# Kernel optimization log

Measured on AMD Instinct MI355X. Metric: run time of the kernel, lower is better.

## Reference

```python
import jax, jax.numpy as jnp
import numpy as np

X_LB, X_UB = 0.0, 25.0  # module-level normalization bounds (time domain)


def _lstm_layer(x, h0, c0, Wih, Whh, bih, bhh):
    """Unbatched PyTorch-style LSTM layer. x: [T, in], returns h seq [T, H].
    Gate order i, f, g, o; gates = x@Wih.T + bih + h@Whh.T + bhh."""
    gx = x @ Wih.T + (bih + bhh)  # [T, 4H] precomputed input contribution

    def step(carry, g):
        h, c = carry
        i, f, gg, o = jnp.split(g + h @ Whh.T, 4)
        c = jax.nn.sigmoid(f) * c + jax.nn.sigmoid(i) * jnp.tanh(gg)
        h = jax.nn.sigmoid(o) * jnp.tanh(c)
        return (h, c), h

    _, hs = jax.lax.scan(step, (h0, c0), gx)
    return hs


def setup_inputs() -> dict:
    key = jax.random.key(0)
    ks = jax.random.split(key, 17)
    T, H1, H2 = 200000, 32, 3

    def u(k, shape, fan):  # torch LSTM default init: U(-1/sqrt(H), 1/sqrt(H))
        s = 1.0 / np.sqrt(fan)
        return jax.random.uniform(k, shape, jnp.float32, -s, s)

    return {
        "x": jax.random.uniform(ks[0], (T, 1), jnp.float32, 0.0, 25.0),
        "pre_Wih0": u(ks[1], (4 * H1, 1), H1),
        "pre_Whh0": u(ks[2], (4 * H1, H1), H1),
        "pre_bih0": u(ks[3], (4 * H1,), H1),
        "pre_bhh0": u(ks[4], (4 * H1,), H1),
        "pre_Wih1": u(ks[5], (4 * H1, H1), H1),
        "pre_Whh1": u(ks[6], (4 * H1, H1), H1),
        "pre_bih1": u(ks[7], (4 * H1,), H1),
        "pre_bhh1": u(ks[8], (4 * H1,), H1),
        "pre_h0": jax.random.normal(ks[9], (2, H1), jnp.float32),
        "pre_c0": jax.random.normal(ks[10], (2, H1), jnp.float32),
        "post_Wih": u(ks[11], (4 * H2, H1), H2),
        "post_Whh": u(ks[12], (4 * H2, H2), H2),
        "post_bih": u(ks[13], (4 * H2,), H2),
        "post_bhh": u(ks[14], (4 * H2,), H2),
        "post_h0": jax.random.normal(ks[15], (1, H2), jnp.float32),
        "post_c0": jax.random.normal(ks[16], (1, H2), jnp.float32),
    }


def reference(x, pre_Wih0, pre_Whh0, pre_bih0, pre_bhh0,
              pre_Wih1, pre_Whh1, pre_bih1, pre_bhh1, pre_h0, pre_c0,
              post_Wih, post_Whh, post_bih, post_bhh, post_h0, post_c0):
    xn = (x - X_LB) / (X_UB - X_LB)                      # input normalization
    h = _lstm_layer(xn, pre_h0[0], pre_c0[0], pre_Wih0, pre_Whh0, pre_bih0, pre_bhh0)
    h = _lstm_layer(h, pre_h0[1], pre_c0[1], pre_Wih1, pre_Whh1, pre_bih1, pre_bhh1)
    out = _lstm_layer(h, post_h0[0], post_c0[0], post_Wih, post_Whh, post_bih, post_bhh)
    return out  # [T, 3]
```

## Files before the change

kernel.cpp:

```cpp
#include <hip/hip_runtime.h>
#include <cstddef>


#define XCH 256
#define SPB 8

typedef float f32x2 __attribute__((ext_vector_type(2)));
typedef float f32x4 __attribute__((ext_vector_type(4)));

__device__ __forceinline__ f32x2 pk_fma(f32x2 a, f32x2 b, f32x2 c) {
    f32x2 d;
    asm("v_pk_fma_f32 %0, %1, %2, %3" : "=v"(d) : "v"(a), "v"(b), "v"(c));
    return d;
}
__device__ __forceinline__ f32x4 lds_ld4(const float* p) {
    f32x4 v; __builtin_memcpy(&v, p, sizeof(f32x4)); return v;
}
__device__ __forceinline__ f32x2 lo2(f32x4 v) { f32x2 r; r[0] = v[0]; r[1] = v[1]; return r; }
__device__ __forceinline__ f32x2 hi2(f32x4 v) { f32x2 r; r[0] = v[2]; r[1] = v[3]; return r; }

__device__ __forceinline__ float v_exp2(float x) {
    float r; asm("v_exp_f32 %0, %1" : "=v"(r) : "v"(x)); return r;
}
__device__ __forceinline__ float v_rcp(float x) {
    float r; asm("v_rcp_f32 %0, %1" : "=v"(r) : "v"(x)); return r;
}
__device__ __forceinline__ float fast_gate_k(float x, float kl2e, float kl2e_lo,
                                             float m, float a0) {
    const float LN2 = 0.69314718055994530942f;
    const float t  = x * kl2e;
    const float r  = fmaf(x, kl2e, -t);
    const float dt = fmaf(x, kl2e_lo, r);
    const float e0 = v_exp2(t);
    const float e  = fmaf(e0, dt * LN2, e0);
    return fmaf(m, v_rcp(1.0f + e), a0);
}
#define KT   (-2.88539004325866699218750f)
#define KT_LO (-3.8519259822e-8f)
__device__ __forceinline__ float fast_tanh(float c) {
    return fast_gate_k(c, KT, KT_LO, 2.0f, -1.0f);
}
#define K1   (-1.44269502162933349609375f)
#define K1_LO (-1.9259629911e-8f)

__device__ __forceinline__ float swap1(float v) {
    return __shfl_xor(v, 1);
}

__device__ __forceinline__ void pipe_barrier() {
    asm volatile("s_waitcnt lgkmcnt(0)\n\ts_barrier" ::: "memory");
}

__global__ __launch_bounds__(256, 1)
void lstm3_r12_kernel(const float* __restrict__ x,
                      const float* __restrict__ Wih0, const float* __restrict__ Whh0,
                      const float* __restrict__ bih0, const float* __restrict__ bhh0,
                      const float* __restrict__ Wih1, const float* __restrict__ Whh1,
                      const float* __restrict__ bih1, const float* __restrict__ bhh1,
                      const float* __restrict__ pre_h0, const float* __restrict__ pre_c0,
                      const float* __restrict__ Wih2, const float* __restrict__ Whh2,
                      const float* __restrict__ bih2, const float* __restrict__ bhh2,
                      const float* __restrict__ post_h0, const float* __restrict__ post_c0,
                      float* __restrict__ out, int T)
{
    const int tid = threadIdx.x;
    const int w   = tid >> 6;
    const int l   = tid & 63;

    __shared__ __align__(16) float h0s[2][SPB][32];
    __shared__ __align__(16) float h1s[2][SPB][32];
    __shared__ __align__(16) float u1s[2][SPB][128];
    __shared__ __align__(16) float xbuf[2][XCH];

    const int T8   = (T + SPB - 1) / SPB;
    const int Etot = T8 + 3;

    if (w == 0) {
        const int cell = l >> 1, hf = l & 1;
        const int rA = cell + (hf << 5);
        const int rB = rA + 64;
        const float wx0A = Wih0[rA];
        const float wx0B = Wih0[rB];
        const float b0A  = bih0[rA] + bhh0[rA];
        const float b0B  = bih0[rB] + bhh0[rB];
        f32x2 wA2[16], wB2[16];
#pragma unroll
        for (int r = 0; r < 16; ++r) {
            wA2[r][0] = Whh0[rA * 32 + 2 * r]; wA2[r][1] = Whh0[rA * 32 + 2 * r + 1];
            wB2[r][0] = Whh0[rB * 32 + 2 * r]; wB2[r][1] = Whh0[rB * 32 + 2 * r + 1];
        }
        const float klB   = (hf == 0) ? KT    : K1;
        const float klBlo = (hf == 0) ? KT_LO : K1_LO;
        const float mB    = (hf == 0) ?  2.0f :  1.0f;
        const float a0B   = (hf == 0) ? -1.0f :  0.0f;

        float c0 = 0.0f;
        if (hf == 0) { c0 = pre_c0[cell]; h0s[1][SPB - 1][cell] = pre_h0[cell]; }
        __syncthreads();

        for (int e = 0; e < Etot; ++e) {
#pragma unroll
            for (int j = 0; j < SPB; ++j) {
                const int t = SPB * e + j;
                const float xn = xbuf[(t >> 8) & 1][t & (XCH - 1)];
                const float* hp = (j == 0) ? h0s[(e + 1) & 1][SPB - 1]
                                           : h0s[e & 1][j - 1];
                f32x2 aA0, aA1, aB0, aB1;
                aA0[0] = fmaf(xn, wx0A, b0A); aA0[1] = 0.0f;
                aA1[0] = 0.0f;                aA1[1] = 0.0f;
                aB0[0] = fmaf(xn, wx0B, b0B); aB0[1] = 0.0f;
                aB1[0] = 0.0f;                aB1[1] = 0.0f;
#pragma unroll
                for (int q = 0; q < 4; ++q) {
                    const f32x4 ha = lds_ld4(&hp[q * 8]);
                    const f32x4 hb = lds_ld4(&hp[q * 8 + 4]);
                    aA0 = pk_fma(lo2(ha), wA2[4 * q],     aA0);
                    aA1 = pk_fma(hi2(ha), wA2[4 * q + 1], aA1);
                    aB0 = pk_fma(lo2(ha), wB2[4 * q],     aB0);
                    aB1 = pk_fma(hi2(ha), wB2[4 * q + 1], aB1);
                    aA0 = pk_fma(lo2(hb), wA2[4 * q + 2], aA0);
                    aA1 = pk_fma(hi2(hb), wA2[4 * q + 3], aA1);
                    aB0 = pk_fma(lo2(hb), wB2[4 * q + 2], aB0);
                    aB1 = pk_fma(hi2(hb), wB2[4 * q + 3], aB1);
                }
                const float sA = (aA0[0] + aA0[1]) + (aA1[0] + aA1[1]);
                const float sB = (aB0[0] + aB0[1]) + (aB1[0] + aB1[1]);
                const float actA = fast_gate_k(sA, K1, K1_LO, 1.0f, 0.0f);
                const float actB = fast_gate_k(sB, klB, klBlo, mB, a0B);
                const float foA = swap1(actA);
                const float foB = swap1(actB);
                if (hf == 0) {
                    c0 = fmaf(foA, c0, actA * actB);
                    h0s[e & 1][j][cell] = foB * fast_tanh(c0);
                }
            }
            pipe_barrier();
        }
    } else if (w == 1) {
        const int gA = l, gB = l + 64;
        const float b1A = bih1[gA] + bhh1[gA];
        f32x2 wA2[16], wB2[16];
#pragma unroll
        for (int r = 0; r < 16; ++r) {
            wA2[r][0] = Wih1[gA * 32 + 2 * r]; wA2[r][1] = Wih1[gA * 32 + 2 * r + 1];
            wB2[r][0] = Wih1[gB * 32 + 2 * r]; wB2[r][1] = Wih1[gB * 32 + 2 * r + 1];
        }
        __syncthreads();

        for (int e = 0; e < Etot; ++e) {
            if (e >= 1) {
#pragma unroll
                for (int j = 0; j < SPB; ++j) {
                    const float* hp = h0s[(e - 1) & 1][j];
                    f32x2 uA0, uA1, uB0, uB1;
                    uA0[0] = b1A;  uA0[1] = 0.0f;
                    uA1[0] = 0.0f; uA1[1] = 0.0f;
                    uB0[0] = 0.0f; uB0[1] = 0.0f;
                    uB1[0] = 0.0f; uB1[1] = 0.0f;
#pragma unroll
                    for (int q = 0; q < 4; ++q) {
                        const f32x4 ha = lds_ld4(&hp[q * 8]);
                        const f32x4 hb = lds_ld4(&hp[q * 8 + 4]);
                        uA0 = pk_fma(lo2(ha), wA2[4 * q],     uA0);
                        uA1 = pk_fma(hi2(ha), wA2[4 * q + 1], uA1);
                        uB0 = pk_fma(lo2(ha), wB2[4 * q],     uB0);
                        uB1 = pk_fma(hi2(ha), wB2[4 * q + 1], uB1);
                        uA0 = pk_fma(lo2(hb), wA2[4 * q + 2], uA0);
                        uA1 = pk_fma(hi2(hb), wA2[4 * q + 3], uA1);
                        uB0 = pk_fma(lo2(hb), wB2[4 * q + 2], uB0);
                        uB1 = pk_fma(hi2(hb), wB2[4 * q + 3], uB1);
                    }
                    f32x2 up;
                    up[0] = (uA0[0] + uA0[1]) + (uA1[0] + uA1[1]);
                    up[1] = (uB0[0] + uB0[1]) + (uB1[0] + uB1[1]);
                    __builtin_memcpy(&u1s[e & 1][j][2 * l], &up, sizeof(f32x2));
                }
            }
            pipe_barrier();
        }
    } else if (w == 2) {
        const int cell = l >> 1, hf = l & 1;
        const int rA = cell + (hf << 5);
        const int rB = rA + 64;
        const float b1B = bih1[rB] + bhh1[rB];
        f32x2 wA2[16], wB2[16];
#pragma unroll
        for (int r = 0; r < 16; ++r) {
            wA2[r][0] = Whh1[rA * 32 + 2 * r]; wA2[r][1] = Whh1[rA * 32 + 2 * r + 1];
            wB2[r][0] = Whh1[rB * 32 + 2 * r]; wB2[r][1] = Whh1[rB * 32 + 2 * r + 1];
        }
        const float klB   = (hf == 0) ? KT    : K1;
        const float klBlo = (hf == 0) ? KT_LO : K1_LO;
        const float mB    = (hf == 0) ?  2.0f :  1.0f;
        const float a0B   = (hf == 0) ? -1.0f :  0.0f;

        float c1 = 0.0f;
        if (hf == 0) { c1 = pre_c0[32 + cell]; h1s[1][SPB - 1][cell] = pre_h0[32 + cell]; }
        __syncthreads();

        for (int e = 0; e < Etot; ++e) {
            if (e >= 2) {
#pragma unroll
                for (int j = 0; j < SPB; ++j) {
                    const float* gp = (j == 0) ? h1s[(e + 1) & 1][SPB - 1]
                                               : h1s[e & 1][j - 1];
                    const f32x4 ga0 = lds_ld4(&gp[0]);
                    const f32x4 gb0 = lds_ld4(&gp[4]);
                    f32x2 Up;
                    __builtin_memcpy(&Up, &u1s[(e - 1) & 1][j][2 * rA], sizeof(f32x2));
                    f32x2 vA0, vA1, vB0, vB1;
                    vA0[0] = 0.0f; vA0[1] = 0.0f;
                    vA1[0] = 0.0f; vA1[1] = 0.0f;
                    vB0[0] = b1B;  vB0[1] = 0.0f;
                    vB1[0] = 0.0f; vB1[1] = 0.0f;
                    vA0 = pk_fma(lo2(ga0), wA2[0], vA0);
                    vA1 = pk_fma(hi2(ga0), wA2[1], vA1);
                    vB0 = pk_fma(lo2(ga0), wB2[0], vB0);
                    vB1 = pk_fma(hi2(ga0), wB2[1], vB1);
                    vA0 = pk_fma(lo2(gb0), wA2[2], vA0);
                    vA1 = pk_fma(hi2(gb0), wA2[3], vA1);
                    vB0 = pk_fma(lo2(gb0), wB2[2], vB0);
                    vB1 = pk_fma(hi2(gb0), wB2[3], vB1);
#pragma unroll
                    for (int q = 1; q < 4; ++q) {
                        const f32x4 ga = lds_ld4(&gp[q * 8]);
                        const f32x4 gb = lds_ld4(&gp[q * 8 + 4]);
                        vA0 = pk_fma(lo2(ga), wA2[4 * q],     vA0);
                        vA1 = pk_fma(hi2(ga), wA2[4 * q + 1], vA1);
                        vB0 = pk_fma(lo2(ga), wB2[4 * q],     vB0);
                        vB1 = pk_fma(hi2(ga), wB2[4 * q + 1], vB1);
                        vA0 = pk_fma(lo2(gb), wA2[4 * q + 2], vA0);
                        vA1 = pk_fma(hi2(gb), wA2[4 * q + 3], vA1);
                        vB0 = pk_fma(lo2(gb), wB2[4 * q + 2], vB0);
                        vB1 = pk_fma(hi2(gb), wB2[4 * q + 3], vB1);
                    }
                    const float sA = Up[0] + ((vA0[0] + vA0[1]) + (vA1[0] + vA1[1]));
                    const float sB = Up[1] + ((vB0[0] + vB0[1]) + (vB1[0] + vB1[1]));
                    const float actA = fast_gate_k(sA, K1, K1_LO, 1.0f, 0.0f);
                    const float actB = fast_gate_k(sB, klB, klBlo, mB, a0B);
                    const float foA = swap1(actA);
                    const float foB = swap1(actB);
                    if (hf == 0) {
                        c1 = fmaf(foA, c1, actA * actB);
                        h1s[e & 1][j][cell] = foB * fast_tanh(c1);
                    }
                }
            }
            pipe_barrier();
        }
    } else {
        const int g2 = (l < 48) ? (l >> 2) : 0;
        const int p  = l & 3;
        f32x2 w2p[4];
#pragma unroll
        for (int r = 0; r < 4; ++r) {
            w2p[r][0] = Wih2[g2 * 32 + p * 8 + 2 * r];
            w2p[r][1] = Wih2[g2 * 32 + p * 8 + 2 * r + 1];
        }
        float wr2[3];
#pragma unroll
        for (int r = 0; r < 3; ++r) wr2[r] = Whh2[g2 * 3 + r];
        const float b2 = bih2[g2] + bhh2[g2];
        const bool  g2tanh = (g2 >= 6 && g2 <= 8);
        const float kl2   = g2tanh ? KT    : K1;
        const float kl2lo = g2tanh ? KT_LO : K1_LO;
        const float m2    = g2tanh ?  2.0f :  1.0f;
        const float a02   = g2tanh ? -1.0f :  0.0f;

        float c2 = 0.0f;
        if (l < 3) c2 = post_c0[l];
        float h2p0 = post_h0[0], h2p1 = post_h0[1], h2p2 = post_h0[2];
        float h2v = 0.0f;

        {
            const int i0 = 4 * l;
            if (i0 < T) {
                const float* xp = x + i0;
                float4 v;
                v.x = xp[0] / 25.0f;
                v.y = (i0 + 1 < T) ? xp[1] / 25.0f : 0.0f;
                v.z = (i0 + 2 < T) ? xp[2] / 25.0f : 0.0f;
                v.w = (i0 + 3 < T) ? xp[3] / 25.0f : 0.0f;
                __builtin_memcpy(&xbuf[0][i0], &v, sizeof(float4));
            }
        }
        __syncthreads();

        for (int e = 0; e < Etot; ++e) {
            if ((e & 31) == 0) {
                const int c = (e >> 5) + 1;
                const int base = c * XCH;
                if (base < T) {
                    const int i0 = base + 4 * l;
                    if (i0 < T) {
                        const float* xp = x + i0;
                        float4 v;
                        v.x = xp[0] / 25.0f;
                        v.y = (i0 + 1 < T) ? xp[1] / 25.0f : 0.0f;
                        v.z = (i0 + 2 < T) ? xp[2] / 25.0f : 0.0f;
                        v.w = (i0 + 3 < T) ? xp[3] / 25.0f : 0.0f;
                        __builtin_memcpy(&xbuf[c & 1][4 * l], &v, sizeof(float4));
                    }
                }
            }
            if (e >= 3) {
#pragma unroll
                for (int j = 0; j < SPB; ++j) {
                    const int t = SPB * (e - 3) + j;
                    const float* hp = h1s[(e - 1) & 1][j];
                    f32x2 acc; acc[0] = 0.0f; acc[1] = 0.0f;
                    {
                        const f32x4 ha = lds_ld4(&hp[p * 8 + 0]);
                        const f32x4 hb = lds_ld4(&hp[p * 8 + 4]);
                        acc = pk_fma(lo2(ha), w2p[0], acc);
                        acc = pk_fma(hi2(ha), w2p[1], acc);
                        acc = pk_fma(lo2(hb), w2p[2], acc);
                        acc = pk_fma(hi2(hb), w2p[3], acc);
                    }
                    float a2 = acc[0] + acc[1];
                    a2 += __shfl_xor(a2, 1);
                    a2 += __shfl_xor(a2, 2);
                    const float rec = fmaf(wr2[2], h2p2,
                                      fmaf(wr2[1], h2p1,
                                      fmaf(wr2[0], h2p0, b2)));
                    a2 += rec;
                    const float act2 = fast_gate_k(a2, kl2, kl2lo, m2, a02);
                    const int lj = (l < 3) ? l : 0;
                    const float i2  = __shfl(act2,  4 * lj);
                    const float f2  = __shfl(act2, 12 + 4 * lj);
                    const float g2v = __shfl(act2, 24 + 4 * lj);
                    const float o2  = __shfl(act2, 36 + 4 * lj);
                    if (l < 3) {
                        c2 = fmaf(f2, c2, i2 * g2v);
                        h2v = o2 * fast_tanh(c2);
                        if (t < T) out[(size_t)t * 3 + l] = h2v;
                    }
                    h2p0 = __shfl(h2v, 0);
                    h2p1 = __shfl(h2v, 1);
                    h2p2 = __shfl(h2v, 2);
                }
            }
            pipe_barrier();
        }
    }
}

extern "C" void kernel_launch(void* const* d_in, const int* in_sizes, int n_in,
                              void* d_out, int out_size, void* d_ws, size_t ws_size,
                              hipStream_t stream)
{
    const float* x       = (const float*)d_in[0];
    const float* Wih0    = (const float*)d_in[1];
    const float* Whh0    = (const float*)d_in[2];
    const float* bih0    = (const float*)d_in[3];
    const float* bhh0    = (const float*)d_in[4];
    const float* Wih1    = (const float*)d_in[5];
    const float* Whh1    = (const float*)d_in[6];
    const float* bih1    = (const float*)d_in[7];
    const float* bhh1    = (const float*)d_in[8];
    const float* pre_h0  = (const float*)d_in[9];
    const float* pre_c0  = (const float*)d_in[10];
    const float* Wih2    = (const float*)d_in[11];
    const float* Whh2    = (const float*)d_in[12];
    const float* bih2    = (const float*)d_in[13];
    const float* bhh2    = (const float*)d_in[14];
    const float* post_h0 = (const float*)d_in[15];
    const float* post_c0 = (const float*)d_in[16];

    const int T = in_sizes[0];

    lstm3_r12_kernel<<<dim3(1), dim3(256), 0, stream>>>(
        x, Wih0, Whh0, bih0, bhh0, Wih1, Whh1, bih1, bhh1, pre_h0, pre_c0,
        Wih2, Whh2, bih2, bhh2, post_h0, post_c0, (float*)d_out, T);
}
```

Before: 57.50 ms.

## Shorten LSTM recurrence critical path with wider accumulators, DPP gate gather, fused o*tanh

Several latency-oriented changes to the sequential single-block LSTM pipeline. Layer 0 and layer 1 now split their dot products across four packed accumulators instead of two, which shortens FMA dependency chains. Layer 0 loads eight x values per epoch with two vector LDS reads, and layer 1 hoists the u1s loads out of the step loop. The output layer is remapped so each of 12 lanes computes a full 32-wide dot product, replacing the cross-lane shuffle reduction and using DPP row shifts to gather gates. The o*tanh(c) product is folded into the final FMA; the DPP row-shift path relies on the 12 gates staying within one 16-lane row.

```diff
diff --git a/kernel.cpp b/kernel.cpp
--- a/kernel.cpp
+++ b/kernel.cpp
@@ -25,34 +25,52 @@
 __device__ __forceinline__ float v_rcp(float x) {
     float r; asm("v_rcp_f32 %0, %1" : "=v"(r) : "v"(x)); return r;
 }
+
+#define LN2F  0.69314718055994530942f
+#define KT    (-2.88539004325866699218750f)
+#define KT_LO (-3.8519259822e-8f)
+#define K1    (-1.44269502162933349609375f)
+#define K1_LO (-1.9259629911e-8f)
+
 __device__ __forceinline__ float fast_gate_k(float x, float kl2e, float kl2e_lo,
                                              float m, float a0) {
-    const float LN2 = 0.69314718055994530942f;
     const float t  = x * kl2e;
     const float r  = fmaf(x, kl2e, -t);
     const float dt = fmaf(x, kl2e_lo, r);
     const float e0 = v_exp2(t);
-    const float e  = fmaf(e0, dt * LN2, e0);
+    const float e  = fmaf(e0, dt * LN2F, e0);
     return fmaf(m, v_rcp(1.0f + e), a0);
 }
-#define KT   (-2.88539004325866699218750f)
-#define KT_LO (-3.8519259822e-8f)
-__device__ __forceinline__ float fast_tanh(float c) {
-    return fast_gate_k(c, KT, KT_LO, 2.0f, -1.0f);
-}
-#define K1   (-1.44269502162933349609375f)
-#define K1_LO (-1.9259629911e-8f)
+__device__ __forceinline__ float o_tanh(float o, float c) {
+    const float t  = c * KT;
+    const float r  = fmaf(c, KT, -t);
+    const float dt = fmaf(c, KT_LO, r);
+    const float e0 = v_exp2(t);
+    const float e  = fmaf(e0, dt * LN2F, e0);
+    const float s  = v_rcp(1.0f + e);
+    return fmaf(o + o, s, -o);
+}
 
 __device__ __forceinline__ float swap1(float v) {
     return __shfl_xor(v, 1);
 }
+template <int N>
+__device__ __forceinline__ float lane_plusN(float v) {
+#if __has_builtin(__builtin_amdgcn_update_dpp)
+    int i = __builtin_bit_cast(int, v);
+    i = __builtin_amdgcn_update_dpp(0, i, 0x100 + N, 0xF, 0xF, false);
+    return __builtin_bit_cast(float, i);
+#else
+    return __shfl_down(v, N);
+#endif
+}
 
 __device__ __forceinline__ void pipe_barrier() {
     asm volatile("s_waitcnt lgkmcnt(0)\n\ts_barrier" ::: "memory");
 }
 
 __global__ __launch_bounds__(256, 1)
-void lstm3_r12_kernel(const float* __restrict__ x,
+void lstm3_r14_kernel(const float* __restrict__ x,
                       const float* __restrict__ Wih0, const float* __restrict__ Whh0,
                       const float* __restrict__ bih0, const float* __restrict__ bhh0,
                       const float* __restrict__ Wih1, const float* __restrict__ Whh1,
@@ -99,39 +117,45 @@
         __syncthreads();
 
         for (int e = 0; e < Etot; ++e) {
+            const int t0 = SPB * e;
+            const float* xp = &xbuf[(t0 >> 8) & 1][t0 & (XCH - 1)];
+            const f32x4 xa = lds_ld4(xp);
+            const f32x4 xb = lds_ld4(xp + 4);
 #pragma unroll
             for (int j = 0; j < SPB; ++j) {
-                const int t = SPB * e + j;
-                const float xn = xbuf[(t >> 8) & 1][t & (XCH - 1)];
+                const float xn = (j < 4) ? xa[j] : xb[j - 4];
                 const float* hp = (j == 0) ? h0s[(e + 1) & 1][SPB - 1]
                                            : h0s[e & 1][j - 1];
-                f32x2 aA0, aA1, aB0, aB1;
-                aA0[0] = fmaf(xn, wx0A, b0A); aA0[1] = 0.0f;
-                aA1[0] = 0.0f;                aA1[1] = 0.0f;
-                aB0[0] = fmaf(xn, wx0B, b0B); aB0[1] = 0.0f;
-                aB1[0] = 0.0f;                aB1[1] = 0.0f;
+                f32x2 aA[4], aB[4];
+                aA[0][0] = fmaf(xn, wx0A, b0A); aA[0][1] = 0.0f;
+                aB[0][0] = fmaf(xn, wx0B, b0B); aB[0][1] = 0.0f;
+#pragma unroll
+                for (int s = 1; s < 4; ++s) { aA[s][0] = 0.0f; aA[s][1] = 0.0f;
+                                              aB[s][0] = 0.0f; aB[s][1] = 0.0f; }
 #pragma unroll
                 for (int q = 0; q < 4; ++q) {
                     const f32x4 ha = lds_ld4(&hp[q * 8]);
                     const f32x4 hb = lds_ld4(&hp[q * 8 + 4]);
-                    aA0 = pk_fma(lo2(ha), wA2[4 * q],     aA0);
-                    aA1 = pk_fma(hi2(ha), wA2[4 * q + 1], aA1);
-                    aB0 = pk_fma(lo2(ha), wB2[4 * q],     aB0);
-                    aB1 = pk_fma(hi2(ha), wB2[4 * q + 1], aB1);
-                    aA0 = pk_fma(lo2(hb), wA2[4 * q + 2], aA0);
-                    aA1 = pk_fma(hi2(hb), wA2[4 * q + 3], aA1);
-                    aB0 = pk_fma(lo2(hb), wB2[4 * q + 2], aB0);
-                    aB1 = pk_fma(hi2(hb), wB2[4 * q + 3], aB1);
-                }
-                const float sA = (aA0[0] + aA0[1]) + (aA1[0] + aA1[1]);
-                const float sB = (aB0[0] + aB0[1]) + (aB1[0] + aB1[1]);
+                    aA[0] = pk_fma(lo2(ha), wA2[4 * q],     aA[0]);
+                    aA[1] = pk_fma(hi2(ha), wA2[4 * q + 1], aA[1]);
+                    aA[2] = pk_fma(lo2(hb), wA2[4 * q + 2], aA[2]);
+                    aA[3] = pk_fma(hi2(hb), wA2[4 * q + 3], aA[3]);
+                    aB[0] = pk_fma(lo2(ha), wB2[4 * q],     aB[0]);
+                    aB[1] = pk_fma(hi2(ha), wB2[4 * q + 1], aB[1]);
+                    aB[2] = pk_fma(lo2(hb), wB2[4 * q + 2], aB[2]);
+                    aB[3] = pk_fma(hi2(hb), wB2[4 * q + 3], aB[3]);
+                }
+                const f32x2 sAv = (aA[0] + aA[1]) + (aA[2] + aA[3]);
+                const f32x2 sBv = (aB[0] + aB[1]) + (aB[2] + aB[3]);
+                const float sA = sAv[0] + sAv[1];
+                const float sB = sBv[0] + sBv[1];
                 const float actA = fast_gate_k(sA, K1, K1_LO, 1.0f, 0.0f);
                 const float actB = fast_gate_k(sB, klB, klBlo, mB, a0B);
                 const float foA = swap1(actA);
                 const float foB = swap1(actB);
                 if (hf == 0) {
                     c0 = fmaf(foA, c0, actA * actB);
-                    h0s[e & 1][j][cell] = foB * fast_tanh(c0);
+                    h0s[e & 1][j][cell] = o_tanh(foB, c0);
                 }
             }
             pipe_barrier();
@@ -200,72 +224,66 @@
 
         for (int e = 0; e < Etot; ++e) {
             if (e >= 2) {
+                f32x2 Up[SPB];
+#pragma unroll
+                for (int j = 0; j < SPB; ++j)
+                    __builtin_memcpy(&Up[j], &u1s[(e - 1) & 1][j][2 * rA], sizeof(f32x2));
 #pragma unroll
                 for (int j = 0; j < SPB; ++j) {
                     const float* gp = (j == 0) ? h1s[(e + 1) & 1][SPB - 1]
                                                : h1s[e & 1][j - 1];
-                    const f32x4 ga0 = lds_ld4(&gp[0]);
-                    const f32x4 gb0 = lds_ld4(&gp[4]);
-                    f32x2 Up;
-                    __builtin_memcpy(&Up, &u1s[(e - 1) & 1][j][2 * rA], sizeof(f32x2));
-                    f32x2 vA0, vA1, vB0, vB1;
-                    vA0[0] = 0.0f; vA0[1] = 0.0f;
-                    vA1[0] = 0.0f; vA1[1] = 0.0f;
-                    vB0[0] = b1B;  vB0[1] = 0.0f;
-                    vB1[0] = 0.0f; vB1[1] = 0.0f;
-                    vA0 = pk_fma(lo2(ga0), wA2[0], vA0);
-                    vA1 = pk_fma(hi2(ga0), wA2[1], vA1);
-                    vB0 = pk_fma(lo2(ga0), wB2[0], vB0);
-                    vB1 = pk_fma(hi2(ga0), wB2[1], vB1);
-                    vA0 = pk_fma(lo2(gb0), wA2[2], vA0);
-                    vA1 = pk_fma(hi2(gb0), wA2[3], vA1);
-                    vB0 = pk_fma(lo2(gb0), wB2[2], vB0);
-                    vB1 = pk_fma(hi2(gb0), wB2[3], vB1);
-#pragma unroll
-                    for (int q = 1; q < 4; ++q) {
+                    f32x2 vA[4], vB[4];
+                    vB[0][0] = b1B;  vB[0][1] = 0.0f;
+                    vA[0][0] = 0.0f; vA[0][1] = 0.0f;
+#pragma unroll
+                    for (int s = 1; s < 4; ++s) { vA[s][0] = 0.0f; vA[s][1] = 0.0f;
+                                                  vB[s][0] = 0.0f; vB[s][1] = 0.0f; }
+#pragma unroll
+                    for (int q = 0; q < 4; ++q) {
                         const f32x4 ga = lds_ld4(&gp[q * 8]);
                         const f32x4 gb = lds_ld4(&gp[q * 8 + 4]);
-                        vA0 = pk_fma(lo2(ga), wA2[4 * q],     vA0);
-                        vA1 = pk_fma(hi2(ga), wA2[4 * q + 1], vA1);
-                        vB0 = pk_fma(lo2(ga), wB2[4 * q],     vB0);
-                        vB1 = pk_fma(hi2(ga), wB2[4 * q + 1], vB1);
-                        vA0 = pk_fma(lo2(gb), wA2[4 * q + 2], vA0);
-                        vA1 = pk_fma(hi2(gb), wA2[4 * q + 3], vA1);
-                        vB0 = pk_fma(lo2(gb), wB2[4 * q + 2], vB0);
-                        vB1 = pk_fma(hi2(gb), wB2[4 * q + 3], vB1);
-                    }
-                    const float sA = Up[0] + ((vA0[0] + vA0[1]) + (vA1[0] + vA1[1]));
-                    const float sB = Up[1] + ((vB0[0] + vB0[1]) + (vB1[0] + vB1[1]));
+                        vA[0] = pk_fma(lo2(ga), wA2[4 * q],     vA[0]);
+                        vA[1] = pk_fma(hi2(ga), wA2[4 * q + 1], vA[1]);
+                        vA[2] = pk_fma(lo2(gb), wA2[4 * q + 2], vA[2]);
+                        vA[3] = pk_fma(hi2(gb), wA2[4 * q + 3], vA[3]);
+                        vB[0] = pk_fma(lo2(ga), wB2[4 * q],     vB[0]);
+                        vB[1] = pk_fma(hi2(ga), wB2[4 * q + 1], vB[1]);
+                        vB[2] = pk_fma(lo2(gb), wB2[4 * q + 2], vB[2]);
+                        vB[3] = pk_fma(hi2(gb), wB2[4 * q + 3], vB[3]);
+                    }
+                    const f32x2 sAv = (vA[0] + vA[1]) + (vA[2] + vA[3]);
+                    const f32x2 sBv = (vB[0] + vB[1]) + (vB[2] + vB[3]);
+                    const float sA = Up[j][0] + (sAv[0] + sAv[1]);
+                    const float sB = Up[j][1] + (sBv[0] + sBv[1]);
                     const float actA = fast_gate_k(sA, K1, K1_LO, 1.0f, 0.0f);
                     const float actB = fast_gate_k(sB, klB, klBlo, mB, a0B);
                     const float foA = swap1(actA);
                     const float foB = swap1(actB);
                     if (hf == 0) {
                         c1 = fmaf(foA, c1, actA * actB);
-                        h1s[e & 1][j][cell] = foB * fast_tanh(c1);
+                        h1s[e & 1][j][cell] = o_tanh(foB, c1);
                     }
                 }
             }
             pipe_barrier();
         }
     } else {
-        const int g2 = (l < 48) ? (l >> 2) : 0;
-        const int p  = l & 3;
-        f32x2 w2p[4];
-#pragma unroll
-        for (int r = 0; r < 4; ++r) {
-            w2p[r][0] = Wih2[g2 * 32 + p * 8 + 2 * r];
-            w2p[r][1] = Wih2[g2 * 32 + p * 8 + 2 * r + 1];
+        const int g = (l < 12) ? l : 0;
+        f32x2 w2[16];
+#pragma unroll
+        for (int r = 0; r < 16; ++r) {
+            w2[r][0] = Wih2[g * 32 + 2 * r];
+            w2[r][1] = Wih2[g * 32 + 2 * r + 1];
         }
         float wr2[3];
 #pragma unroll
-        for (int r = 0; r < 3; ++r) wr2[r] = Whh2[g2 * 3 + r];
-        const float b2 = bih2[g2] + bhh2[g2];
-        const bool  g2tanh = (g2 >= 6 && g2 <= 8);
-        const float kl2   = g2tanh ? KT    : K1;
-        const float kl2lo = g2tanh ? KT_LO : K1_LO;
-        const float m2    = g2tanh ?  2.0f :  1.0f;
-        const float a02   = g2tanh ? -1.0f :  0.0f;
+        for (int r = 0; r < 3; ++r) wr2[r] = Whh2[g * 3 + r];
+        const float b2 = bih2[g] + bhh2[g];
+        const bool  gt = (g >= 6 && g <= 8);
+        const float kl2   = gt ? KT    : K1;
+        const float kl2lo = gt ? KT_LO : K1_LO;
+        const float m2    = gt ?  2.0f :  1.0f;
+        const float a02   = gt ? -1.0f :  0.0f;
 
         float c2 = 0.0f;
         if (l < 3) c2 = post_c0[l];
@@ -308,31 +326,30 @@
                 for (int j = 0; j < SPB; ++j) {
                     const int t = SPB * (e - 3) + j;
                     const float* hp = h1s[(e - 1) & 1][j];
-                    f32x2 acc; acc[0] = 0.0f; acc[1] = 0.0f;
-                    {
-                        const f32x4 ha = lds_ld4(&hp[p * 8 + 0]);
-                        const f32x4 hb = lds_ld4(&hp[p * 8 + 4]);
-                        acc = pk_fma(lo2(ha), w2p[0], acc);
-                        acc = pk_fma(hi2(ha), w2p[1], acc);
-                        acc = pk_fma(lo2(hb), w2p[2], acc);
-                        acc = pk_fma(hi2(hb), w2p[3], acc);
-                    }
-                    float a2 = acc[0] + acc[1];
-                    a2 += __shfl_xor(a2, 1);
-                    a2 += __shfl_xor(a2, 2);
-                    const float rec = fmaf(wr2[2], h2p2,
-                                      fmaf(wr2[1], h2p1,
-                                      fmaf(wr2[0], h2p0, b2)));
-                    a2 += rec;
+                    f32x2 ac[4];
+#pragma unroll
+                    for (int s = 0; s < 4; ++s) { ac[s][0] = 0.0f; ac[s][1] = 0.0f; }
+#pragma unroll
+                    for (int q = 0; q < 4; ++q) {
+                        const f32x4 ha = lds_ld4(&hp[q * 8]);
+                        const f32x4 hb = lds_ld4(&hp[q * 8 + 4]);
+                        ac[0] = pk_fma(lo2(ha), w2[4 * q],     ac[0]);
+                        ac[1] = pk_fma(hi2(ha), w2[4 * q + 1], ac[1]);
+                        ac[2] = pk_fma(lo2(hb), w2[4 * q + 2], ac[2]);
+                        ac[3] = pk_fma(hi2(hb), w2[4 * q + 3], ac[3]);
+                    }
+                    const f32x2 sv = (ac[0] + ac[1]) + (ac[2] + ac[3]);
+                    float a2 = sv[0] + sv[1];
+                    a2 += fmaf(wr2[2], h2p2,
+                          fmaf(wr2[1], h2p1,
+                          fmaf(wr2[0], h2p0, b2)));
                     const float act2 = fast_gate_k(a2, kl2, kl2lo, m2, a02);
-                    const int lj = (l < 3) ? l : 0;
-                    const float i2  = __shfl(act2,  4 * lj);
-                    const float f2  = __shfl(act2, 12 + 4 * lj);
-                    const float g2v = __shfl(act2, 24 + 4 * lj);
-                    const float o2  = __shfl(act2, 36 + 4 * lj);
+                    const float f2  = lane_plusN<3>(act2);
+                    const float g2v = lane_plusN<6>(act2);
+                    const float o2  = lane_plusN<9>(act2);
                     if (l < 3) {
-                        c2 = fmaf(f2, c2, i2 * g2v);
-                        h2v = o2 * fast_tanh(c2);
+                        c2 = fmaf(f2, c2, act2 * g2v);
+                        h2v = o_tanh(o2, c2);
                         if (t < T) out[(size_t)t * 3 + l] = h2v;
                     }
                     h2p0 = __shfl(h2v, 0);
@@ -369,7 +386,7 @@
 
     const int T = in_sizes[0];
 
-    lstm3_r12_kernel<<<dim3(1), dim3(256), 0, stream>>>(
+    lstm3_r14_kernel<<<dim3(1), dim3(256), 0, stream>>>(
         x, Wih0, Whh0, bih0, bhh0, Wih1, Whh1, bih1, bhh1, pre_h0, pre_c0,
         Wih2, Whh2, bih2, bhh2, post_h0, post_c0, (float*)d_out, T);
 }
```

Measured after the change: 56.43 ms. Within noise of the previous version (-1.9%).
